# Kernel tuning notes

Hardware: AMD Instinct MI355X
Metric: run time of the kernel (lower is better)

Reference implementation:

```python
import jax, jax.numpy as jnp
import numpy as np


def _gather_neighbors(v, idx):
    # v: [B, N, D], idx: [B, N, K] -> [B, N, K, D]
    return jax.vmap(lambda vb, ib: vb[ib])(v, idx)


def setup_inputs() -> dict:
    key = jax.random.key(0)
    B, N, P, D, K = 8, 2048, 64, 128, 16
    ks = jax.random.split(key, 24)
    s = lambda fan_in: 1.0 / np.sqrt(fan_in)
    inp = {
        "x": jax.random.normal(ks[0], (B, N, 3), jnp.float32),
        "in_f": jax.random.normal(ks[1], (B, N, P), jnp.float32),
        "W_fc1": jax.random.normal(ks[2], (P, D), jnp.float32) * s(P),
        "b_fc1": jnp.zeros((D,), jnp.float32),
        "W_phi": jax.random.normal(ks[3], (D, D), jnp.float32) * s(D),
        "W_psi": jax.random.normal(ks[4], (D, D), jnp.float32) * s(D),
        "W_alpha": jax.random.normal(ks[5], (D, D), jnp.float32) * s(D),
        "W_dpt1": jax.random.normal(ks[6], (D, D), jnp.float32) * s(D),
        "b_dpt1": jnp.zeros((D,), jnp.float32),
        "W_dpt2": jax.random.normal(ks[7], (D, D), jnp.float32) * s(D),
        "b_dpt2": jnp.zeros((D,), jnp.float32),
        "W_gam1": jax.random.normal(ks[8], (D, D), jnp.float32) * s(D),
        "b_gam1": jnp.zeros((D,), jnp.float32),
        "W_gam2": jax.random.normal(ks[9], (D, D), jnp.float32) * s(D),
        "b_gam2": jnp.zeros((D,), jnp.float32),
        "W_del1": jax.random.normal(ks[10], (3, D), jnp.float32) * s(3),
        "b_del1": jnp.zeros((D,), jnp.float32),
        "W_del2": jax.random.normal(ks[11], (D, D), jnp.float32) * s(D),
        "b_del2": jnp.zeros((D,), jnp.float32),
        "W_fc2": jax.random.normal(ks[12], (D, P), jnp.float32) * s(D),
        "b_fc2": jnp.zeros((P,), jnp.float32),
        "k": K,
    }
    return inp


def reference(x, in_f, W_fc1, b_fc1, W_phi, W_psi, W_alpha,
              W_dpt1, b_dpt1, W_dpt2, b_dpt2,
              W_gam1, b_gam1, W_gam2, b_gam2,
              W_del1, b_del1, W_del2, b_del2,
              W_fc2, b_fc2, k):
    # squared pairwise distance [B, N, N] without [B,N,N,3] intermediate
    x2 = jnp.sum(x * x, axis=-1)                      # [B, N]
    d2 = x2[:, :, None] + x2[:, None, :] - 2.0 * jnp.einsum('bnc,bmc->bnm', x, x)
    knn_idx = jnp.argsort(d2, axis=-1)[:, :, :k]       # [B, N, K]

    points_knn = _gather_neighbors(x, knn_idx)         # [B, N, K, 3]
    f = in_f @ W_fc1 + b_fc1                           # [B, N, D]

    # positional encoding delta: MLP(x_i - x_j)
    diff = x[:, :, None, :] - points_knn               # [B, N, K, 3]
    delta = jax.nn.relu(diff @ W_del1 + b_del1) @ W_del2 + b_del2  # [B,N,K,D]

    psi = _gather_neighbors(f @ W_psi, knn_idx)        # [B, N, K, D]
    phi = (f @ W_phi)[:, :, None, :]                   # [B, N, 1, D]
    alpha = _gather_neighbors(f @ W_alpha, knn_idx)    # [B, N, K, D]
    dropped = (jax.nn.relu(f @ W_dpt1 + b_dpt1) @ W_dpt2 + b_dpt2)[:, :, None, :]

    pre = phi - psi + delta + dropped                  # [B, N, K, D]
    gamma = jax.nn.relu(pre @ W_gam1 + b_gam1) @ W_gam2 + b_gam2
    rho = jax.nn.softmax(gamma / jnp.sqrt(jnp.float32(k)), axis=2)

    y = jnp.sum(rho * (alpha + delta), axis=2)         # [B, N, D]
    return y @ W_fc2 + b_fc2 + in_f
```

## Files before the change

### kernel.cpp

```cpp
#include <hip/hip_runtime.h>
#include <hip/hip_bf16.h>
#include <math.h>

#define Bq 8
#define Nq 2048
#define Pq 64
#define Dq 128
#define Kq 16
#define BNq (Bq * Nq)

typedef unsigned short u16;
typedef __bf16 bf16x8v __attribute__((ext_vector_type(8)));
typedef float f32x4v __attribute__((ext_vector_type(4)));

__device__ __forceinline__ u16 f2b(float f) {
    return __builtin_bit_cast(u16, (__bf16)f);
}

#define OFF_DEL2 0
#define OFF_GAM1 16384
#define OFF_GAM2 32768
#define OFF_FC1  49152
#define OFF_PHI  57344
#define OFF_PSI  73728
#define OFF_ALF  90112
#define OFF_DPT1 106496
#define OFF_DPT2 122880
#define WT_TOTAL 139264

__global__ __launch_bounds__(256) void prep_kernel(
    const float* __restrict__ Wdel2, const float* __restrict__ Wgam1,
    const float* __restrict__ Wgam2, const float* __restrict__ Wfc1,
    const float* __restrict__ Wphi, const float* __restrict__ Wpsi,
    const float* __restrict__ Walpha, const float* __restrict__ Wdpt1,
    const float* __restrict__ Wdpt2, u16* __restrict__ Wt) {
    int idx = blockIdx.x * 256 + threadIdx.x;
    const float* W;
    int n, k;
    if (idx < OFF_FC1) {
        int m = idx >> 14, r = idx & 16383;
        W = (m == 0) ? Wdel2 : (m == 1) ? Wgam1 : Wgam2;
        n = r >> 7; k = r & 127;
    } else if (idx < OFF_PHI) {
        int r = idx - OFF_FC1;
        W = Wfc1; n = r >> 6; k = r & 63;
    } else {
        int r = idx - OFF_PHI;
        int m = r >> 14; r &= 16383;
        W = (m == 0) ? Wphi : (m == 1) ? Wpsi : (m == 2) ? Walpha : (m == 3) ? Wdpt1 : Wdpt2;
        n = r >> 7; k = r & 127;
    }
    Wt[idx] = f2b(W[k * 128 + n]);
}

__global__ __launch_bounds__(256) void knn_kernel(const float* __restrict__ x,
                                                  int* __restrict__ knn) {
    __shared__ float4 sx[Nq];
    __shared__ float sLd[32][8][17];
    __shared__ int   sLi[32][8][17];
    const int b = blockIdx.x >> 6;
    const int q0 = (blockIdx.x & 63) * 32;
    const float* xb = x + b * Nq * 3;
    for (int j = threadIdx.x; j < Nq; j += 256) {
        float x0 = xb[j * 3 + 0], x1 = xb[j * 3 + 1], x2 = xb[j * 3 + 2];
        float n2 = __fadd_rn(__fadd_rn(__fmul_rn(x0, x0), __fmul_rn(x1, x1)),
                             __fmul_rn(x2, x2));
        sx[j] = make_float4(x0, x1, x2, n2);
    }
    __syncthreads();
    const int q = threadIdx.x & 31;
    const int sub = threadIdx.x >> 5;
    const float4 qv = sx[q0 + q];
    float bd[Kq];
    int bj[Kq];
#pragma unroll
    for (int s = 0; s < Kq; ++s) { bd[s] = INFINITY; bj[s] = 0; }
    const int j0 = sub * 256;
    for (int i = 0; i < 256; ++i) {
        const int j = j0 + i;
        float4 p = sx[j];
        float dot = __fadd_rn(__fadd_rn(__fmul_rn(qv.x, p.x), __fmul_rn(qv.y, p.y)),
                              __fmul_rn(qv.z, p.z));
        float d = __fsub_rn(__fadd_rn(qv.w, p.w), __fmul_rn(2.0f, dot));
        if (d < bd[Kq - 1]) {
            bd[Kq - 1] = d; bj[Kq - 1] = j;
#pragma unroll
            for (int s = Kq - 1; s >= 1; --s) {
                if (bd[s] < bd[s - 1]) {
                    float td = bd[s]; bd[s] = bd[s - 1]; bd[s - 1] = td;
                    int tj = bj[s]; bj[s] = bj[s - 1]; bj[s - 1] = tj;
                }
            }
        }
    }
#pragma unroll
    for (int s = 0; s < Kq; ++s) { sLd[q][sub][s] = bd[s]; sLi[q][sub][s] = bj[s]; }
    __syncthreads();
    if (threadIdx.x < 32) {
        const int mq = threadIdx.x;
        int pos[8]; float hd[8]; int hi[8];
#pragma unroll
        for (int s = 0; s < 8; ++s) {
            pos[s] = 1; hd[s] = sLd[mq][s][0]; hi[s] = sLi[mq][s][0];
        }
        int* o = knn + (b * Nq + q0 + mq) * Kq;
#pragma unroll
        for (int oi = 0; oi < Kq; ++oi) {
            float bdv = hd[0]; int biv = hi[0]; int bs = 0;
#pragma unroll
            for (int s = 1; s < 8; ++s) {
                bool take = (hd[s] < bdv) || (hd[s] == bdv && hi[s] < biv);
                if (take) { bdv = hd[s]; biv = hi[s]; bs = s; }
            }
            o[oi] = biv;
#pragma unroll
            for (int s = 0; s < 8; ++s) {
                if (s == bs) {
                    int pp = pos[s] < Kq ? pos[s] : (Kq - 1);
                    bool ok = pos[s] < Kq;
                    hd[s] = ok ? sLd[mq][s][pp] : INFINITY;
                    hi[s] = ok ? sLi[mq][s][pp] : 0x7fffffff;
                    pos[s]++;
                }
            }
        }
    }
}

template <int BYTES, int ROWBYTES>
__device__ __forceinline__ void stageW(const u16* __restrict__ src,
                                       u16* __restrict__ sW, int t) {
#pragma unroll
    for (int c = 0; c < BYTES / 4096; ++c) {
        int lin = c * 4096 + t * 16;
        int n = lin / ROWBYTES;
        int o = lin % ROWBYTES;
        bf16x8v v = *(const bf16x8v*)((const char*)src + lin);
        *(bf16x8v*)((char*)sW + n * ROWBYTES + (o ^ ((n & 7) << 4))) = v;
    }
}

__device__ __forceinline__ void mfma_k128(const u16* __restrict__ sA,
                                          const u16* __restrict__ sW,
                                          int colbase, int lane,
                                          f32x4v (&acc)[4][2]) {
    const int kg = lane >> 4;
    const int l15 = lane & 15;
#pragma unroll
    for (int ks = 0; ks < 4; ++ks) {
        bf16x8v a[4], bfr[2];
#pragma unroll
        for (int m = 0; m < 4; ++m) {
            int row = m * 16 + l15;
            int o = (ks * 64 + kg * 16) ^ ((row & 7) << 4);
            a[m] = *(const bf16x8v*)((const char*)sA + row * 256 + o);
        }
#pragma unroll
        for (int nt = 0; nt < 2; ++nt) {
            int n = colbase + nt * 16 + l15;
            int o = (ks * 64 + kg * 16) ^ ((n & 7) << 4);
            bfr[nt] = *(const bf16x8v*)((const char*)sW + n * 256 + o);
        }
#pragma unroll
        for (int m = 0; m < 4; ++m)
#pragma unroll
            for (int nt = 0; nt < 2; ++nt)
                acc[m][nt] = __builtin_amdgcn_mfma_f32_16x16x32_bf16(a[m], bfr[nt], acc[m][nt], 0, 0, 0);
    }
}

__device__ __forceinline__ void mfma_k64(const u16* __restrict__ sA,
                                         const u16* __restrict__ sW,
                                         int colbase, int lane,
                                         f32x4v (&acc)[4][2]) {
    const int kg = lane >> 4;
    const int l15 = lane & 15;
#pragma unroll
    for (int ks = 0; ks < 2; ++ks) {
        bf16x8v a[4], bfr[2];
#pragma unroll
        for (int m = 0; m < 4; ++m) {
            int row = m * 16 + l15;
            int o = (ks * 64 + kg * 16) ^ ((row & 7) << 4);
            a[m] = *(const bf16x8v*)((const char*)sA + row * 128 + o);
        }
#pragma unroll
        for (int nt = 0; nt < 2; ++nt) {
            int n = colbase + nt * 16 + l15;
            int o = (ks * 64 + kg * 16) ^ ((n & 7) << 4);
            bfr[nt] = *(const bf16x8v*)((const char*)sW + n * 128 + o);
        }
#pragma unroll
        for (int m = 0; m < 4; ++m)
#pragma unroll
            for (int nt = 0; nt < 2; ++nt)
                acc[m][nt] = __builtin_amdgcn_mfma_f32_16x16x32_bf16(a[m], bfr[nt], acc[m][nt], 0, 0, 0);
    }
}

__global__ __launch_bounds__(256, 2) void feat_kernel(
    const float* __restrict__ in_f, const u16* __restrict__ Wt,
    const float* __restrict__ bfc1, const float* __restrict__ bdpt1,
    const float* __restrict__ bdpt2,
    float* __restrict__ base, u16* __restrict__ psiB, u16* __restrict__ alphaB) {
    __shared__ __align__(16) u16 sIn[64 * 64];
    __shared__ __align__(16) u16 sF[64 * 128];
    __shared__ __align__(16) u16 sW[128 * 128];
    const int t = threadIdx.x;
    const int lane = t & 63;
    const int w = t >> 6;
    const int kg = lane >> 4;
    const int l15 = lane & 15;
    const int p0 = blockIdx.x * 64;

    {
        const int r = t >> 2;
        const int c0 = (t & 3) * 16;
        const float* src = &in_f[(size_t)(p0 + r) * 64 + c0];
        float4 v0 = *(const float4*)(src + 0);
        float4 v1 = *(const float4*)(src + 4);
        float4 v2 = *(const float4*)(src + 8);
        float4 v3 = *(const float4*)(src + 12);
        bf16x8v lo, hi;
        lo[0] = (__bf16)v0.x; lo[1] = (__bf16)v0.y; lo[2] = (__bf16)v0.z; lo[3] = (__bf16)v0.w;
        lo[4] = (__bf16)v1.x; lo[5] = (__bf16)v1.y; lo[6] = (__bf16)v1.z; lo[7] = (__bf16)v1.w;
        hi[0] = (__bf16)v2.x; hi[1] = (__bf16)v2.y; hi[2] = (__bf16)v2.z; hi[3] = (__bf16)v2.w;
        hi[4] = (__bf16)v3.x; hi[5] = (__bf16)v3.y; hi[6] = (__bf16)v3.z; hi[7] = (__bf16)v3.w;
        const int swz = (r & 7) << 4;
        *(bf16x8v*)((char*)sIn + r * 128 + ((c0 * 2) ^ swz)) = lo;
        *(bf16x8v*)((char*)sIn + r * 128 + (((c0 + 8) * 2) ^ swz)) = hi;
    }

    f32x4v acc[4][2], accPhi[4][2];

    {
        float bv0 = bfc1[w * 32 + l15];
        float bv1 = bfc1[w * 32 + 16 + l15];
#pragma unroll
        for (int m = 0; m < 4; ++m) { acc[m][0] = f32x4v{bv0, bv0, bv0, bv0}; acc[m][1] = f32x4v{bv1, bv1, bv1, bv1}; }
    }
    stageW<16384, 128>(Wt + OFF_FC1, sW, t);
    __syncthreads();
    mfma_k64(sIn, sW, w * 32, lane, acc);

#pragma unroll
    for (int m = 0; m < 4; ++m)
#pragma unroll
        for (int nt = 0; nt < 2; ++nt)
#pragma unroll
            for (int rr = 0; rr < 4; ++rr) {
                int row = m * 16 + kg * 4 + rr;
                int col = w * 32 + nt * 16 + l15;
                *(__bf16*)((char*)sF + row * 256 + ((col * 2) ^ ((row & 7) << 4))) = (__bf16)acc[m][nt][rr];
            }

#pragma unroll
    for (int m = 0; m < 4; ++m) { accPhi[m][0] = f32x4v{0, 0, 0, 0}; accPhi[m][1] = f32x4v{0, 0, 0, 0}; }
    __syncthreads();
    stageW<32768, 256>(Wt + OFF_PHI, sW, t);
    __syncthreads();
    mfma_k128(sF, sW, w * 32, lane, accPhi);

#pragma unroll
    for (int m = 0; m < 4; ++m) { acc[m][0] = f32x4v{0, 0, 0, 0}; acc[m][1] = f32x4v{0, 0, 0, 0}; }
    __syncthreads();
    stageW<32768, 256>(Wt + OFF_PSI, sW, t);
    __syncthreads();
    mfma_k128(sF, sW, w * 32, lane, acc);
#pragma unroll
    for (int m = 0; m < 4; ++m)
#pragma unroll
        for (int nt = 0; nt < 2; ++nt)
#pragma unroll
            for (int rr = 0; rr < 4; ++rr) {
                int row = m * 16 + kg * 4 + rr;
                int col = w * 32 + nt * 16 + l15;
                psiB[(size_t)(p0 + row) * 128 + col] = f2b(acc[m][nt][rr]);
            }

#pragma unroll
    for (int m = 0; m < 4; ++m) { acc[m][0] = f32x4v{0, 0, 0, 0}; acc[m][1] = f32x4v{0, 0, 0, 0}; }
    __syncthreads();
    stageW<32768, 256>(Wt + OFF_ALF, sW, t);
    __syncthreads();
    mfma_k128(sF, sW, w * 32, lane, acc);
#pragma unroll
    for (int m = 0; m < 4; ++m)
#pragma unroll
        for (int nt = 0; nt < 2; ++nt)
#pragma unroll
            for (int rr = 0; rr < 4; ++rr) {
                int row = m * 16 + kg * 4 + rr;
                int col = w * 32 + nt * 16 + l15;
                alphaB[(size_t)(p0 + row) * 128 + col] = f2b(acc[m][nt][rr]);
            }

    {
        float bv0 = bdpt1[w * 32 + l15];
        float bv1 = bdpt1[w * 32 + 16 + l15];
#pragma unroll
        for (int m = 0; m < 4; ++m) { acc[m][0] = f32x4v{bv0, bv0, bv0, bv0}; acc[m][1] = f32x4v{bv1, bv1, bv1, bv1}; }
    }
    __syncthreads();
    stageW<32768, 256>(Wt + OFF_DPT1, sW, t);
    __syncthreads();
    mfma_k128(sF, sW, w * 32, lane, acc);
    __syncthreads();
#pragma unroll
    for (int m = 0; m < 4; ++m)
#pragma unroll
        for (int nt = 0; nt < 2; ++nt)
#pragma unroll
            for (int rr = 0; rr < 4; ++rr) {
                int row = m * 16 + kg * 4 + rr;
                int col = w * 32 + nt * 16 + l15;
                *(__bf16*)((char*)sF + row * 256 + ((col * 2) ^ ((row & 7) << 4))) =
                    (__bf16)fmaxf(acc[m][nt][rr], 0.f);
            }

    {
        float bv0 = bdpt2[w * 32 + l15];
        float bv1 = bdpt2[w * 32 + 16 + l15];
#pragma unroll
        for (int m = 0; m < 4; ++m) { acc[m][0] = f32x4v{bv0, bv0, bv0, bv0}; acc[m][1] = f32x4v{bv1, bv1, bv1, bv1}; }
    }
    __syncthreads();
    stageW<32768, 256>(Wt + OFF_DPT2, sW, t);
    __syncthreads();
    mfma_k128(sF, sW, w * 32, lane, acc);
#pragma unroll
    for (int m = 0; m < 4; ++m)
#pragma unroll
        for (int nt = 0; nt < 2; ++nt)
#pragma unroll
            for (int rr = 0; rr < 4; ++rr) {
                int row = m * 16 + kg * 4 + rr;
                int col = w * 32 + nt * 16 + l15;
                base[(size_t)(p0 + row) * 128 + col] = acc[m][nt][rr] + accPhi[m][nt][rr];
            }
}

__device__ __forceinline__ void do_stage(const u16* __restrict__ Wt_stage,
                                         const u16* sA, u16* sW,
                                         int t, int w, int lane,
                                         f32x4v (&acc)[4][2]) {
    __syncthreads();
    stageW<32768, 256>(Wt_stage, sW, t);
    __syncthreads();
    mfma_k128(sA, sW, w * 32, lane, acc);
}

__global__ __launch_bounds__(256, 2) void main_kernel(
    const float* __restrict__ x, const float* __restrict__ in_f,
    const float* __restrict__ Wdel1, const float* __restrict__ bdel1,
    const float* __restrict__ bdel2,
    const float* __restrict__ bgam1, const float* __restrict__ bgam2,
    const float* __restrict__ Wfc2, const float* __restrict__ bfc2,
    const float* __restrict__ base, const u16* __restrict__ psiB,
    const u16* __restrict__ alphaB, const int* __restrict__ knn,
    const u16* __restrict__ Wt, float* __restrict__ out) {
    __shared__ __align__(16) u16 sA[64 * 128];
    __shared__ __align__(16) u16 sBP[64 * 128];
    __shared__ __align__(16) u16 sW[128 * 128];
    __shared__ float sWd1[512];
    __shared__ float sDiff[64][3];
    __shared__ int sIdx[64];
    __shared__ float sY[4][128];

    const int t = threadIdx.x;
    const int lane = t & 63;
    const int w = t >> 6;
    const int kg = lane >> 4;
    const int l15 = lane & 15;
    const int p0 = blockIdx.x * 4;
    const int b = p0 >> 11;

    if (t < 64) {
        int p = p0 + (t >> 4);
        int j = knn[p * Kq + (t & 15)];
        sIdx[t] = b * Nq + j;
        const float* xq = x + p * 3;
        const float* xn = x + ((size_t)(b * Nq + j)) * 3;
        sDiff[t][0] = xq[0] - xn[0];
        sDiff[t][1] = xq[1] - xn[1];
        sDiff[t][2] = xq[2] - xn[2];
    }
#pragma unroll
    for (int i = 0; i < 2; ++i) {
        int idx = t + i * 256;
        sWd1[idx] = (idx < 384) ? Wdel1[idx] : bdel1[idx - 384];
    }
    __syncthreads();

    const int r = t >> 2;
    const int cb = t & 3;
    const float dx = sDiff[r][0], dy = sDiff[r][1], dz = sDiff[r][2];
    const int nrow = sIdx[r];
    const int prow = p0 + (r >> 4);
    bf16x8v aStash[4];
#pragma unroll
    for (int c8 = 0; c8 < 4; ++c8) {
        const int col0 = cb * 32 + c8 * 8;
        const int obyte = (col0 * 2) ^ ((r & 7) << 4);
        bf16x8v hv;
#pragma unroll
        for (int j = 0; j < 8; ++j) {
            int cc = col0 + j;
            float v = fmaf(dz, sWd1[256 + cc], fmaf(dy, sWd1[128 + cc], fmaf(dx, sWd1[cc], sWd1[384 + cc])));
            hv[j] = (__bf16)fmaxf(v, 0.f);
        }
        *(bf16x8v*)((char*)sA + r * 256 + obyte) = hv;
        bf16x8v ps = *(const bf16x8v*)&psiB[(size_t)nrow * 128 + col0];
        float4 b0 = *(const float4*)&base[(size_t)prow * 128 + col0];
        float4 b1 = *(const float4*)&base[(size_t)prow * 128 + col0 + 4];
        bf16x8v bp;
        bp[0] = (__bf16)(b0.x - (float)ps[0]); bp[1] = (__bf16)(b0.y - (float)ps[1]);
        bp[2] = (__bf16)(b0.z - (float)ps[2]); bp[3] = (__bf16)(b0.w - (float)ps[3]);
        bp[4] = (__bf16)(b1.x - (float)ps[4]); bp[5] = (__bf16)(b1.y - (float)ps[5]);
        bp[6] = (__bf16)(b1.z - (float)ps[6]); bp[7] = (__bf16)(b1.w - (float)ps[7]);
        *(bf16x8v*)((char*)sBP + r * 256 + obyte) = bp;
        aStash[c8] = *(const bf16x8v*)&alphaB[(size_t)nrow * 128 + col0];
    }

    f32x4v accD[4][2], accW[4][2];
    {
        float bv0 = bdel2[w * 32 + l15];
        float bv1 = bdel2[w * 32 + 16 + l15];
#pragma unroll
        for (int m = 0; m < 4; ++m) { accD[m][0] = f32x4v{bv0, bv0, bv0, bv0}; accD[m][1] = f32x4v{bv1, bv1, bv1, bv1}; }
    }
    do_stage(Wt + OFF_DEL2, sA, sW, t, w, lane, accD);
    __syncthreads();

#pragma unroll
    for (int m = 0; m < 4; ++m)
#pragma unroll
        for (int nt = 0; nt < 2; ++nt)
#pragma unroll
            for (int rr = 0; rr < 4; ++rr) {
                int row = m * 16 + kg * 4 + rr;
                int col = w * 32 + nt * 16 + l15;
                int off = row * 256 + ((col * 2) ^ ((row & 7) << 4));
                float bp = (float)*(const __bf16*)((const char*)sBP + off);
                *(__bf16*)((char*)sA + off) = (__bf16)(accD[m][nt][rr] + bp);
            }
    __syncthreads();

#pragma unroll
    for (int c8 = 0; c8 < 4; ++c8) {
        const int col0 = cb * 32 + c8 * 8;
        *(bf16x8v*)((char*)sBP + r * 256 + ((col0 * 2) ^ ((r & 7) << 4))) = aStash[c8];
    }

    {
        float bv0 = bgam1[w * 32 + l15];
        float bv1 = bgam1[w * 32 + 16 + l15];
#pragma unroll
        for (int m = 0; m < 4; ++m) { accW[m][0] = f32x4v{bv0, bv0, bv0, bv0}; accW[m][1] = f32x4v{bv1, bv1, bv1, bv1}; }
    }
    do_stage(Wt + OFF_GAM1, sA, sW, t, w, lane, accW);
    __syncthreads();

#pragma unroll
    for (int m = 0; m < 4; ++m)
#pragma unroll
        for (int nt = 0; nt < 2; ++nt)
#pragma unroll
            for (int rr = 0; rr < 4; ++rr) {
                int row = m * 16 + kg * 4 + rr;
                int col = w * 32 + nt * 16 + l15;
                int off = row * 256 + ((col * 2) ^ ((row & 7) << 4));
                *(__bf16*)((char*)sA + off) = (__bf16)fmaxf(accW[m][nt][rr], 0.f);
            }

    {
        float bv0 = bgam2[w * 32 + l15];
        float bv1 = bgam2[w * 32 + 16 + l15];
#pragma unroll
        for (int m = 0; m < 4; ++m) { accW[m][0] = f32x4v{bv0, bv0, bv0, bv0}; accW[m][1] = f32x4v{bv1, bv1, bv1, bv1}; }
    }
    do_stage(Wt + OFF_GAM2, sA, sW, t, w, lane, accW);

#pragma unroll
    for (int m = 0; m < 4; ++m)
#pragma unroll
        for (int nt = 0; nt < 2; ++nt) {
            const int col = w * 32 + nt * 16 + l15;
            float g0 = accW[m][nt][0], g1v = accW[m][nt][1], g2 = accW[m][nt][2], g3 = accW[m][nt][3];
            float mx = fmaxf(fmaxf(g0, g1v), fmaxf(g2, g3));
            mx = fmaxf(mx, __shfl_xor(mx, 16, 64));
            mx = fmaxf(mx, __shfl_xor(mx, 32, 64));
            float m4 = mx * 0.25f;
            float e0 = expf(0.25f * g0 - m4), e1 = expf(0.25f * g1v - m4);
            float e2 = expf(0.25f * g2 - m4), e3 = expf(0.25f * g3 - m4);
            float s = e0 + e1 + e2 + e3;
            s += __shfl_xor(s, 16, 64);
            s += __shfl_xor(s, 32, 64);
            float y = 0.f;
#pragma unroll
            for (int rr = 0; rr < 4; ++rr) {
                int row = m * 16 + kg * 4 + rr;
                int off = row * 256 + ((col * 2) ^ ((row & 7) << 4));
                float al = (float)*(const __bf16*)((const char*)sBP + off);
                float ev = (rr == 0) ? e0 : (rr == 1) ? e1 : (rr == 2) ? e2 : e3;
                y = fmaf(ev, al + accD[m][nt][rr], y);
            }
            y += __shfl_xor(y, 16, 64);
            y += __shfl_xor(y, 32, 64);
            if (kg == 0) sY[m][col] = y / s;
        }
    __syncthreads();

    {
        const int p = t >> 6;
        const int q = t & 63;
        const int gp = p0 + p;
        float a = bfc2[q] + in_f[(size_t)gp * 64 + q];
#pragma unroll 8
        for (int d = 0; d < 128; ++d)
            a = fmaf(sY[p][d], Wfc2[d * 64 + q], a);
        out[(size_t)gp * 64 + q] = a;
    }
}

extern "C" void kernel_launch(void* const* d_in, const int* in_sizes, int n_in,
                              void* d_out, int out_size, void* d_ws, size_t ws_size,
                              hipStream_t stream) {
    const float* x     = (const float*)d_in[0];
    const float* in_f  = (const float*)d_in[1];
    const float* Wfc1  = (const float*)d_in[2];
    const float* bfc1  = (const float*)d_in[3];
    const float* Wphi  = (const float*)d_in[4];
    const float* Wpsi  = (const float*)d_in[5];
    const float* Walpha= (const float*)d_in[6];
    const float* Wdpt1 = (const float*)d_in[7];
    const float* bdpt1 = (const float*)d_in[8];
    const float* Wdpt2 = (const float*)d_in[9];
    const float* bdpt2 = (const float*)d_in[10];
    const float* Wgam1 = (const float*)d_in[11];
    const float* bgam1 = (const float*)d_in[12];
    const float* Wgam2 = (const float*)d_in[13];
    const float* bgam2 = (const float*)d_in[14];
    const float* Wdel1 = (const float*)d_in[15];
    const float* bdel1 = (const float*)d_in[16];
    const float* Wdel2 = (const float*)d_in[17];
    const float* bdel2 = (const float*)d_in[18];
    const float* Wfc2  = (const float*)d_in[19];
    const float* bfc2  = (const float*)d_in[20];
    float* out = (float*)d_out;

    float* base   = (float*)d_ws;
    u16*   psiB   = (u16*)(base + (size_t)BNq * Dq);
    u16*   alphaB = psiB + (size_t)BNq * Dq;
    int*   knn    = (int*)(alphaB + (size_t)BNq * Dq);
    u16*   Wt     = (u16*)(knn + (size_t)BNq * Kq);

    prep_kernel<<<WT_TOTAL / 256, 256, 0, stream>>>(Wdel2, Wgam1, Wgam2, Wfc1, Wphi,
                                                    Wpsi, Walpha, Wdpt1, Wdpt2, Wt);
    knn_kernel<<<512, 256, 0, stream>>>(x, knn);
    feat_kernel<<<BNq / 64, 256, 0, stream>>>(in_f, Wt, bfc1, bdpt1, bdpt2,
                                              base, psiB, alphaB);
    main_kernel<<<BNq / 4, 256, 0, stream>>>(x, in_f, Wdel1, bdel1, bdel2,
                                             bgam1, bgam2, Wfc2, bfc2,
                                             base, psiB, alphaB, knn, Wt, out);
}
```

Before: 238.9 us.

## Persist main kernel over point chunks with resident weights; widen kNN to 512 threads

Result: slower. 290.0 us (+21.4%).

```diff
diff --git a/kernel.cpp b/kernel.cpp
--- a/kernel.cpp
+++ b/kernel.cpp
@@ -53,15 +53,15 @@
     Wt[idx] = f2b(W[k * 128 + n]);
 }
 
-__global__ __launch_bounds__(256) void knn_kernel(const float* __restrict__ x,
+__global__ __launch_bounds__(512) void knn_kernel(const float* __restrict__ x,
                                                   int* __restrict__ knn) {
     __shared__ float4 sx[Nq];
-    __shared__ float sLd[32][8][17];
-    __shared__ int   sLi[32][8][17];
+    __shared__ float sLd[32][16][17];
+    __shared__ u16   sLi[32][16][17];
     const int b = blockIdx.x >> 6;
     const int q0 = (blockIdx.x & 63) * 32;
     const float* xb = x + b * Nq * 3;
-    for (int j = threadIdx.x; j < Nq; j += 256) {
+    for (int j = threadIdx.x; j < Nq; j += 512) {
         float x0 = xb[j * 3 + 0], x1 = xb[j * 3 + 1], x2 = xb[j * 3 + 2];
         float n2 = __fadd_rn(__fadd_rn(__fmul_rn(x0, x0), __fmul_rn(x1, x1)),
                              __fmul_rn(x2, x2));
@@ -74,9 +74,9 @@
     float bd[Kq];
     int bj[Kq];
 #pragma unroll
-    for (int s = 0; s < Kq; ++s) { bd[s] = INFINITY; bj[s] = 0; }
-    const int j0 = sub * 256;
-    for (int i = 0; i < 256; ++i) {
+    for (int s = 0; s < Kq; ++s) { bd[s] = INFINITY; bj[s] = 0x7fff; }
+    const int j0 = sub * 128;
+    for (int i = 0; i < 128; ++i) {
         const int j = j0 + i;
         float4 p = sx[j];
         float dot = __fadd_rn(__fadd_rn(__fmul_rn(qv.x, p.x), __fmul_rn(qv.y, p.y)),
@@ -94,14 +94,31 @@
         }
     }
 #pragma unroll
-    for (int s = 0; s < Kq; ++s) { sLd[q][sub][s] = bd[s]; sLi[q][sub][s] = bj[s]; }
+    for (int s = 0; s < Kq; ++s) { sLd[q][sub][s] = bd[s]; sLi[q][sub][s] = (u16)bj[s]; }
+    __syncthreads();
+    if (threadIdx.x < 256) {
+        const int mq = threadIdx.x & 31;
+        const int s2 = threadIdx.x >> 5;
+        float md[Kq]; int mi[Kq];
+        int pa = 0, pb = 0;
+#pragma unroll
+        for (int i = 0; i < Kq; ++i) {
+            float da = sLd[mq][2 * s2][pa], db = sLd[mq][2 * s2 + 1][pb];
+            int ia = sLi[mq][2 * s2][pa], ib = sLi[mq][2 * s2 + 1][pb];
+            bool ta = (da < db) || (da == db && ia < ib);
+            md[i] = ta ? da : db; mi[i] = ta ? ia : ib;
+            if (ta) ++pa; else ++pb;
+        }
+#pragma unroll
+        for (int i = 0; i < Kq; ++i) { sLd[mq][2 * s2][i] = md[i]; sLi[mq][2 * s2][i] = (u16)mi[i]; }
+    }
     __syncthreads();
     if (threadIdx.x < 32) {
         const int mq = threadIdx.x;
         int pos[8]; float hd[8]; int hi[8];
 #pragma unroll
         for (int s = 0; s < 8; ++s) {
-            pos[s] = 1; hd[s] = sLd[mq][s][0]; hi[s] = sLi[mq][s][0];
+            pos[s] = 1; hd[s] = sLd[mq][2 * s][0]; hi[s] = sLi[mq][2 * s][0];
         }
         int* o = knn + (b * Nq + q0 + mq) * Kq;
 #pragma unroll
@@ -118,8 +135,8 @@
                 if (s == bs) {
                     int pp = pos[s] < Kq ? pos[s] : (Kq - 1);
                     bool ok = pos[s] < Kq;
-                    hd[s] = ok ? sLd[mq][s][pp] : INFINITY;
-                    hi[s] = ok ? sLi[mq][s][pp] : 0x7fffffff;
+                    hd[s] = ok ? sLd[mq][2 * s][pp] : INFINITY;
+                    hi[s] = ok ? sLi[mq][2 * s][pp] : 0x7fffffff;
                     pos[s]++;
                 }
             }
@@ -340,17 +357,30 @@
             }
 }
 
-__device__ __forceinline__ void do_stage(const u16* __restrict__ Wt_stage,
-                                         const u16* sA, u16* sW,
-                                         int t, int w, int lane,
-                                         f32x4v (&acc)[4][2]) {
-    __syncthreads();
-    stageW<32768, 256>(Wt_stage, sW, t);
-    __syncthreads();
-    mfma_k128(sA, sW, w * 32, lane, acc);
-}
-
-__global__ __launch_bounds__(256, 2) void main_kernel(
+__device__ __forceinline__ void mfma_n1(const u16* __restrict__ sA,
+                                        const u16* __restrict__ sW,
+                                        int colW, int kg, int l15,
+                                        f32x4v (&acc)[4]) {
+#pragma unroll
+    for (int ks = 0; ks < 4; ++ks) {
+        bf16x8v a[4], bb;
+#pragma unroll
+        for (int m = 0; m < 4; ++m) {
+            int row = m * 16 + l15;
+            int o = (ks * 64 + kg * 16) ^ ((row & 7) << 4);
+            a[m] = *(const bf16x8v*)((const char*)sA + row * 256 + o);
+        }
+        {
+            int o = (ks * 64 + kg * 16) ^ ((colW & 7) << 4);
+            bb = *(const bf16x8v*)((const char*)sW + colW * 256 + o);
+        }
+#pragma unroll
+        for (int m = 0; m < 4; ++m)
+            acc[m] = __builtin_amdgcn_mfma_f32_16x16x32_bf16(a[m], bb, acc[m], 0, 0, 0);
+    }
+}
+
+__global__ __launch_bounds__(512, 1) void main_kernel(
     const float* __restrict__ x, const float* __restrict__ in_f,
     const float* __restrict__ Wdel1, const float* __restrict__ bdel1,
     const float* __restrict__ bdel2,
@@ -359,10 +389,9 @@
     const float* __restrict__ base, const u16* __restrict__ psiB,
     const u16* __restrict__ alphaB, const int* __restrict__ knn,
     const u16* __restrict__ Wt, float* __restrict__ out) {
+    __shared__ __align__(16) u16 sW3[3][128 * 128];
     __shared__ __align__(16) u16 sA[64 * 128];
     __shared__ __align__(16) u16 sBP[64 * 128];
-    __shared__ __align__(16) u16 sW[128 * 128];
-    __shared__ float sWd1[512];
     __shared__ float sDiff[64][3];
     __shared__ int sIdx[64];
     __shared__ float sY[4][128];
@@ -372,121 +401,130 @@
     const int w = t >> 6;
     const int kg = lane >> 4;
     const int l15 = lane & 15;
-    const int p0 = blockIdx.x * 4;
-    const int b = p0 >> 11;
-
-    if (t < 64) {
-        int p = p0 + (t >> 4);
-        int j = knn[p * Kq + (t & 15)];
-        sIdx[t] = b * Nq + j;
-        const float* xq = x + p * 3;
-        const float* xn = x + ((size_t)(b * Nq + j)) * 3;
-        sDiff[t][0] = xq[0] - xn[0];
-        sDiff[t][1] = xq[1] - xn[1];
-        sDiff[t][2] = xq[2] - xn[2];
-    }
-#pragma unroll
-    for (int i = 0; i < 2; ++i) {
-        int idx = t + i * 256;
-        sWd1[idx] = (idx < 384) ? Wdel1[idx] : bdel1[idx - 384];
-    }
-    __syncthreads();
-
-    const int r = t >> 2;
-    const int cb = t & 3;
-    const float dx = sDiff[r][0], dy = sDiff[r][1], dz = sDiff[r][2];
-    const int nrow = sIdx[r];
-    const int prow = p0 + (r >> 4);
-    bf16x8v aStash[4];
-#pragma unroll
-    for (int c8 = 0; c8 < 4; ++c8) {
-        const int col0 = cb * 32 + c8 * 8;
-        const int obyte = (col0 * 2) ^ ((r & 7) << 4);
-        bf16x8v hv;
-#pragma unroll
-        for (int j = 0; j < 8; ++j) {
-            int cc = col0 + j;
-            float v = fmaf(dz, sWd1[256 + cc], fmaf(dy, sWd1[128 + cc], fmaf(dx, sWd1[cc], sWd1[384 + cc])));
-            hv[j] = (__bf16)fmaxf(v, 0.f);
-        }
-        *(bf16x8v*)((char*)sA + r * 256 + obyte) = hv;
-        bf16x8v ps = *(const bf16x8v*)&psiB[(size_t)nrow * 128 + col0];
-        float4 b0 = *(const float4*)&base[(size_t)prow * 128 + col0];
-        float4 b1 = *(const float4*)&base[(size_t)prow * 128 + col0 + 4];
-        bf16x8v bp;
-        bp[0] = (__bf16)(b0.x - (float)ps[0]); bp[1] = (__bf16)(b0.y - (float)ps[1]);
-        bp[2] = (__bf16)(b0.z - (float)ps[2]); bp[3] = (__bf16)(b0.w - (float)ps[3]);
-        bp[4] = (__bf16)(b1.x - (float)ps[4]); bp[5] = (__bf16)(b1.y - (float)ps[5]);
-        bp[6] = (__bf16)(b1.z - (float)ps[6]); bp[7] = (__bf16)(b1.w - (float)ps[7]);
-        *(bf16x8v*)((char*)sBP + r * 256 + obyte) = bp;
-        aStash[c8] = *(const bf16x8v*)&alphaB[(size_t)nrow * 128 + col0];
-    }
-
-    f32x4v accD[4][2], accW[4][2];
-    {
-        float bv0 = bdel2[w * 32 + l15];
-        float bv1 = bdel2[w * 32 + 16 + l15];
-#pragma unroll
-        for (int m = 0; m < 4; ++m) { accD[m][0] = f32x4v{bv0, bv0, bv0, bv0}; accD[m][1] = f32x4v{bv1, bv1, bv1, bv1}; }
-    }
-    do_stage(Wt + OFF_DEL2, sA, sW, t, w, lane, accD);
-    __syncthreads();
-
-#pragma unroll
-    for (int m = 0; m < 4; ++m)
-#pragma unroll
-        for (int nt = 0; nt < 2; ++nt)
-#pragma unroll
-            for (int rr = 0; rr < 4; ++rr) {
-                int row = m * 16 + kg * 4 + rr;
-                int col = w * 32 + nt * 16 + l15;
-                int off = row * 256 + ((col * 2) ^ ((row & 7) << 4));
-                float bp = (float)*(const __bf16*)((const char*)sBP + off);
-                *(__bf16*)((char*)sA + off) = (__bf16)(accD[m][nt][rr] + bp);
-            }
-    __syncthreads();
-
-#pragma unroll
-    for (int c8 = 0; c8 < 4; ++c8) {
-        const int col0 = cb * 32 + c8 * 8;
-        *(bf16x8v*)((char*)sBP + r * 256 + ((col0 * 2) ^ ((r & 7) << 4))) = aStash[c8];
-    }
-
-    {
-        float bv0 = bgam1[w * 32 + l15];
-        float bv1 = bgam1[w * 32 + 16 + l15];
-#pragma unroll
-        for (int m = 0; m < 4; ++m) { accW[m][0] = f32x4v{bv0, bv0, bv0, bv0}; accW[m][1] = f32x4v{bv1, bv1, bv1, bv1}; }
-    }
-    do_stage(Wt + OFF_GAM1, sA, sW, t, w, lane, accW);
-    __syncthreads();
-
-#pragma unroll
-    for (int m = 0; m < 4; ++m)
-#pragma unroll
-        for (int nt = 0; nt < 2; ++nt)
-#pragma unroll
-            for (int rr = 0; rr < 4; ++rr) {
-                int row = m * 16 + kg * 4 + rr;
-                int col = w * 32 + nt * 16 + l15;
-                int off = row * 256 + ((col * 2) ^ ((row & 7) << 4));
-                *(__bf16*)((char*)sA + off) = (__bf16)fmaxf(accW[m][nt][rr], 0.f);
-            }
-
-    {
-        float bv0 = bgam2[w * 32 + l15];
-        float bv1 = bgam2[w * 32 + 16 + l15];
-#pragma unroll
-        for (int m = 0; m < 4; ++m) { accW[m][0] = f32x4v{bv0, bv0, bv0, bv0}; accW[m][1] = f32x4v{bv1, bv1, bv1, bv1}; }
-    }
-    do_stage(Wt + OFF_GAM2, sA, sW, t, w, lane, accW);
-
-#pragma unroll
-    for (int m = 0; m < 4; ++m)
-#pragma unroll
-        for (int nt = 0; nt < 2; ++nt) {
-            const int col = w * 32 + nt * 16 + l15;
-            float g0 = accW[m][nt][0], g1v = accW[m][nt][1], g2 = accW[m][nt][2], g3 = accW[m][nt][3];
+    const int colW = w * 16 + l15;
+
+#pragma unroll
+    for (int s = 0; s < 3; ++s) {
+        const u16* src = Wt + s * 16384;
+        u16* dst = sW3[s];
+#pragma unroll
+        for (int c = 0; c < 4; ++c) {
+            int lin = c * 8192 + t * 16;
+            int n = lin >> 8;
+            int o = lin & 255;
+            bf16x8v v = *(const bf16x8v*)((const char*)src + lin);
+            *(bf16x8v*)((char*)dst + n * 256 + (o ^ ((n & 7) << 4))) = v;
+        }
+    }
+    const int hr = t >> 3;
+    const int hc0 = (t & 7) * 16;
+    float wdx[16], wdy[16], wdz[16], wdb[16];
+#pragma unroll
+    for (int c = 0; c < 4; ++c) {
+        *(float4*)&wdx[c * 4] = *(const float4*)&Wdel1[0 * 128 + hc0 + c * 4];
+        *(float4*)&wdy[c * 4] = *(const float4*)&Wdel1[1 * 128 + hc0 + c * 4];
+        *(float4*)&wdz[c * 4] = *(const float4*)&Wdel1[2 * 128 + hc0 + c * 4];
+        *(float4*)&wdb[c * 4] = *(const float4*)&bdel1[hc0 + c * 4];
+    }
+    const float bD = bdel2[colW];
+    const float bG1 = bgam1[colW];
+    const float bG2 = bgam2[colW];
+    float bO = 0.f;
+    if (t < 256) bO = bfc2[t & 63];
+
+    const int pbase = blockIdx.x * 64;
+    const int b = pbase >> 11;
+
+    for (int chunk = 0; chunk < 16; ++chunk) {
+        const int p0 = pbase + chunk * 4;
+        if (t < 64) {
+            int p = p0 + (t >> 4);
+            int j = knn[p * Kq + (t & 15)];
+            sIdx[t] = b * Nq + j;
+            const float* xq = x + (size_t)p * 3;
+            const float* xn = x + (size_t)(b * Nq + j) * 3;
+            sDiff[t][0] = xq[0] - xn[0];
+            sDiff[t][1] = xq[1] - xn[1];
+            sDiff[t][2] = xq[2] - xn[2];
+        }
+        __syncthreads();
+
+        bf16x8v aSt[2];
+        {
+            const float dx = sDiff[hr][0], dy = sDiff[hr][1], dz = sDiff[hr][2];
+            const int nrow = sIdx[hr];
+            const int prow = p0 + (hr >> 4);
+            const int swz = (hr & 7) << 4;
+#pragma unroll
+            for (int hh = 0; hh < 2; ++hh) {
+                const int c0 = hc0 + hh * 8;
+                bf16x8v ps = *(const bf16x8v*)&psiB[(size_t)nrow * 128 + c0];
+                float4 b0 = *(const float4*)&base[(size_t)prow * 128 + c0];
+                float4 b1 = *(const float4*)&base[(size_t)prow * 128 + c0 + 4];
+                aSt[hh] = *(const bf16x8v*)&alphaB[(size_t)nrow * 128 + c0];
+                bf16x8v hv, bp;
+#pragma unroll
+                for (int j = 0; j < 8; ++j) {
+                    int c = hh * 8 + j;
+                    float v = fmaf(dz, wdz[c], fmaf(dy, wdy[c], fmaf(dx, wdx[c], wdb[c])));
+                    hv[j] = (__bf16)fmaxf(v, 0.f);
+                }
+                bp[0] = (__bf16)(b0.x - (float)ps[0]); bp[1] = (__bf16)(b0.y - (float)ps[1]);
+                bp[2] = (__bf16)(b0.z - (float)ps[2]); bp[3] = (__bf16)(b0.w - (float)ps[3]);
+                bp[4] = (__bf16)(b1.x - (float)ps[4]); bp[5] = (__bf16)(b1.y - (float)ps[5]);
+                bp[6] = (__bf16)(b1.z - (float)ps[6]); bp[7] = (__bf16)(b1.w - (float)ps[7]);
+                const int ob = ((c0 * 2) ^ swz);
+                *(bf16x8v*)((char*)sA + hr * 256 + ob) = hv;
+                *(bf16x8v*)((char*)sBP + hr * 256 + ob) = bp;
+            }
+        }
+        __syncthreads();
+
+        f32x4v accD[4];
+#pragma unroll
+        for (int m = 0; m < 4; ++m) accD[m] = f32x4v{bD, bD, bD, bD};
+        mfma_n1(sA, sW3[0], colW, kg, l15, accD);
+        __syncthreads();
+
+#pragma unroll
+        for (int m = 0; m < 4; ++m)
+#pragma unroll
+            for (int rr = 0; rr < 4; ++rr) {
+                int row = m * 16 + kg * 4 + rr;
+                int off = row * 256 + ((colW * 2) ^ ((row & 7) << 4));
+                float bpv = (float)*(const __bf16*)((const char*)sBP + off);
+                *(__bf16*)((char*)sA + off) = (__bf16)(accD[m][rr] + bpv);
+            }
+        __syncthreads();
+
+        {
+            const int swz = (hr & 7) << 4;
+            *(bf16x8v*)((char*)sBP + hr * 256 + ((hc0 * 2) ^ swz)) = aSt[0];
+            *(bf16x8v*)((char*)sBP + hr * 256 + (((hc0 + 8) * 2) ^ swz)) = aSt[1];
+        }
+        f32x4v accT[4];
+#pragma unroll
+        for (int m = 0; m < 4; ++m) accT[m] = f32x4v{bG1, bG1, bG1, bG1};
+        mfma_n1(sA, sW3[1], colW, kg, l15, accT);
+        __syncthreads();
+
+#pragma unroll
+        for (int m = 0; m < 4; ++m)
+#pragma unroll
+            for (int rr = 0; rr < 4; ++rr) {
+                int row = m * 16 + kg * 4 + rr;
+                int off = row * 256 + ((colW * 2) ^ ((row & 7) << 4));
+                *(__bf16*)((char*)sA + off) = (__bf16)fmaxf(accT[m][rr], 0.f);
+            }
+        __syncthreads();
+
+#pragma unroll
+        for (int m = 0; m < 4; ++m) accT[m] = f32x4v{bG2, bG2, bG2, bG2};
+        mfma_n1(sA, sW3[2], colW, kg, l15, accT);
+
+#pragma unroll
+        for (int m = 0; m < 4; ++m) {
+            float g0 = accT[m][0], g1v = accT[m][1], g2 = accT[m][2], g3 = accT[m][3];
             float mx = fmaxf(fmaxf(g0, g1v), fmaxf(g2, g3));
             mx = fmaxf(mx, __shfl_xor(mx, 16, 64));
             mx = fmaxf(mx, __shfl_xor(mx, 32, 64));
@@ -500,26 +538,27 @@
 #pragma unroll
             for (int rr = 0; rr < 4; ++rr) {
                 int row = m * 16 + kg * 4 + rr;
-                int off = row * 256 + ((col * 2) ^ ((row & 7) << 4));
+                int off = row * 256 + ((colW * 2) ^ ((row & 7) << 4));
                 float al = (float)*(const __bf16*)((const char*)sBP + off);
                 float ev = (rr == 0) ? e0 : (rr == 1) ? e1 : (rr == 2) ? e2 : e3;
-                y = fmaf(ev, al + accD[m][nt][rr], y);
+                y = fmaf(ev, al + accD[m][rr], y);
             }
             y += __shfl_xor(y, 16, 64);
             y += __shfl_xor(y, 32, 64);
-            if (kg == 0) sY[m][col] = y / s;
-        }
-    __syncthreads();
-
-    {
-        const int p = t >> 6;
-        const int q = t & 63;
-        const int gp = p0 + p;
-        float a = bfc2[q] + in_f[(size_t)gp * 64 + q];
+            if (kg == 0) sY[m][colW] = y / s;
+        }
+        __syncthreads();
+
+        if (t < 256) {
+            const int p = t >> 6;
+            const int q = t & 63;
+            const int gp = p0 + p;
+            float a = bO + in_f[(size_t)gp * 64 + q];
 #pragma unroll 8
-        for (int d = 0; d < 128; ++d)
-            a = fmaf(sY[p][d], Wfc2[d * 64 + q], a);
-        out[(size_t)gp * 64 + q] = a;
+            for (int d = 0; d < 128; ++d)
+                a = fmaf(sY[p][d], Wfc2[d * 64 + q], a);
+            out[(size_t)gp * 64 + q] = a;
+        }
     }
 }
 
@@ -557,10 +596,10 @@
 
     prep_kernel<<<WT_TOTAL / 256, 256, 0, stream>>>(Wdel2, Wgam1, Wgam2, Wfc1, Wphi,
                                                     Wpsi, Walpha, Wdpt1, Wdpt2, Wt);
-    knn_kernel<<<512, 256, 0, stream>>>(x, knn);
+    knn_kernel<<<512, 512, 0, stream>>>(x, knn);
     feat_kernel<<<BNq / 64, 256, 0, stream>>>(in_f, Wt, bfc1, bdpt1, bdpt2,
                                               base, psiB, alphaB);
-    main_kernel<<<BNq / 4, 256, 0, stream>>>(x, in_f, Wdel1, bdel1, bdel2,
-                                             bgam1, bgam2, Wfc2, bfc2,
-                                             base, psiB, alphaB, knn, Wt, out);
-}
+    main_kernel<<<256, 512, 0, stream>>>(x, in_f, Wdel1, bdel1, bdel2,
+                                         bgam1, bgam2, Wfc2, bfc2,
+                                         base, psiB, alphaB, knn, Wt, out);
+}
```
